# Kernel tuning notes

Measured on AMD Instinct MI355X. Metric: run time of the kernel, lower is better.

## Reference

```python
import jax, jax.numpy as jnp
import numpy as np

N, S, C = 2048, 14, 30  # batch, grid, channels (B=2 boxes*5 + 20 classes)
L_COORD, L_NOOBJ = 5.0, 0.5


def setup_inputs() -> dict:
    key = jax.random.key(0)
    k1, k2, k3 = jax.random.split(key, 3)
    pred = jax.random.uniform(k1, (N, S, S, C), minval=0.05, maxval=1.0, dtype=jnp.float32)
    target = jax.random.uniform(k2, (N, S, S, C), minval=0.05, maxval=1.0, dtype=jnp.float32)
    conf = (jax.random.uniform(k3, (N, S, S)) > 0.7).astype(jnp.float32)
    target = target.at[..., 4].set(conf)
    return {"pred": pred, "target": target}


def _to_xyxy(b):
    # b[..., :2] = center (grid units, divided by 14), b[..., 2:4] = w,h (image units)
    xy = b[..., :2] / 14.0
    wh = b[..., 2:4]
    return jnp.concatenate([xy - 0.5 * wh, xy + 0.5 * wh], axis=-1)


def _yolo_loss(pred, target):
    n = pred.shape[0]
    coo = (target[..., 4] > 0).astype(pred.dtype)   # [N,S,S] object mask
    noo = 1.0 - coo                                  # no-object mask
    pb = pred[..., :10].reshape(pred.shape[:3] + (2, 5))    # [N,S,S,2,5]
    tb = target[..., :10].reshape(target.shape[:3] + (2, 5))

    # IoU of the 2 predicted boxes vs the FIRST target box of the cell
    p_xy = _to_xyxy(pb)              # [N,S,S,2,4]
    t_xy = _to_xyxy(tb[..., 0, :])   # [N,S,S,4]
    lt = jnp.maximum(p_xy[..., :2], t_xy[..., None, :2])
    rb = jnp.minimum(p_xy[..., 2:], t_xy[..., None, 2:])
    wh = jnp.clip(rb - lt, 0.0)
    inter = wh[..., 0] * wh[..., 1]                          # [N,S,S,2]
    a1 = (p_xy[..., 2] - p_xy[..., 0]) * (p_xy[..., 3] - p_xy[..., 1])
    a2 = ((t_xy[..., 2] - t_xy[..., 0]) * (t_xy[..., 3] - t_xy[..., 1]))[..., None]
    iou = inter / (a1 + a2 - inter)

    # responsible box = argmax IoU (selection only; IoU value never enters the
    # loss because the original writes max_iou into cols :4 but reads col 4=0)
    r = jnp.argmax(jax.lax.stop_gradient(iou), axis=-1)      # [N,S,S]
    idx = r[..., None, None]
    resp_p = jnp.take_along_axis(pb, idx, axis=3)[..., 0, :]      # [N,S,S,5]
    resp_t = jnp.take_along_axis(tb, idx, axis=3)[..., 0, :]
    nresp_p = jnp.take_along_axis(pb, 1 - idx, axis=3)[..., 0, :]

    cm = coo[..., None]
    loc = jnp.sum(cm * (resp_p[..., :2] - resp_t[..., :2]) ** 2) \
        + jnp.sum(cm * (jnp.sqrt(resp_p[..., 2:4]) - jnp.sqrt(resp_t[..., 2:4])) ** 2)
    contain = jnp.sum(coo * resp_p[..., 4] ** 2)       # target IoU col 4 is 0 in original
    not_contain = jnp.sum(coo * nresp_p[..., 4] ** 2)  # target conf zeroed in original
    noobj = jnp.sum(noo * ((pred[..., 4] - target[..., 4]) ** 2
                           + (pred[..., 9] - target[..., 9]) ** 2))
    cls = jnp.sum(cm * (pred[..., 10:] - target[..., 10:]) ** 2)
    return (L_COORD * loc + 2.0 * contain + not_contain + L_NOOBJ * noobj + cls) / n


def reference(pred, target):
    return _yolo_loss(pred, target)
```

## Files before the change

### kernel.cpp

```cpp
#include <hip/hip_runtime.h>


constexpr int N_IMG = 2048;
constexpr int NC    = 30;
constexpr int CELLS = N_IMG * 14 * 14;
constexpr int BLOCK = 256;
constexpr int CPB   = 256;
constexpr int GRID  = CELLS / CPB;

__global__ __launch_bounds__(BLOCK)
void yolo_partial(const float* __restrict__ pred,
                  const float* __restrict__ targ,
                  float* __restrict__ partial)
{
    __shared__ float sp[CPB * NC];
    __shared__ float st[CPB * NC];
    __shared__ float wsum[BLOCK / 64];

    const int tid = threadIdx.x;
    const size_t base = (size_t)blockIdx.x * (size_t)(CPB * NC);

    const float4* gp = reinterpret_cast<const float4*>(pred + base);
    const float4* gt = reinterpret_cast<const float4*>(targ + base);
    float4* lp = reinterpret_cast<float4*>(sp);
    float4* lt = reinterpret_cast<float4*>(st);
    constexpr int NV = CPB * NC / 4;
    #pragma unroll
    for (int i = 0; i < NV / BLOCK; ++i) {
        lp[tid + i * BLOCK] = gp[tid + i * BLOCK];
        lt[tid + i * BLOCK] = gt[tid + i * BLOCK];
    }
    if (tid < NV - (NV / BLOCK) * BLOCK) {
        const int i = (NV / BLOCK) * BLOCK + tid;
        lp[i] = gp[i];
        lt[i] = gt[i];
    }
    __syncthreads();

    float pv[NC], tv[NC];
    {
        const float2* p2 = reinterpret_cast<const float2*>(sp + tid * NC);
        const float2* t2 = reinterpret_cast<const float2*>(st + tid * NC);
        #pragma unroll
        for (int i = 0; i < NC / 2; ++i) {
            float2 a = p2[i]; pv[2*i] = a.x; pv[2*i+1] = a.y;
            float2 b = t2[i]; tv[2*i] = b.x; tv[2*i+1] = b.y;
        }
    }

    const float coo = (tv[4] > 0.0f) ? 1.0f : 0.0f;

    const float txc = tv[0] / 14.0f, tyc = tv[1] / 14.0f;
    const float tx1 = txc - 0.5f * tv[2], ty1 = tyc - 0.5f * tv[3];
    const float tx2 = txc + 0.5f * tv[2], ty2 = tyc + 0.5f * tv[3];
    const float t_area = (tx2 - tx1) * (ty2 - ty1);

    float iou0, iou1;
    {
        const float xc = pv[0] / 14.0f, yc = pv[1] / 14.0f;
        const float x1 = xc - 0.5f * pv[2], y1 = yc - 0.5f * pv[3];
        const float x2 = xc + 0.5f * pv[2], y2 = yc + 0.5f * pv[3];
        const float a1 = (x2 - x1) * (y2 - y1);
        const float wx = fmaxf(fminf(x2, tx2) - fmaxf(x1, tx1), 0.0f);
        const float wy = fmaxf(fminf(y2, ty2) - fmaxf(y1, ty1), 0.0f);
        const float inter = wx * wy;
        iou0 = inter / (a1 + t_area - inter);
    }
    {
        const float xc = pv[5] / 14.0f, yc = pv[6] / 14.0f;
        const float x1 = xc - 0.5f * pv[7], y1 = yc - 0.5f * pv[8];
        const float x2 = xc + 0.5f * pv[7], y2 = yc + 0.5f * pv[8];
        const float a1 = (x2 - x1) * (y2 - y1);
        const float wx = fmaxf(fminf(x2, tx2) - fmaxf(x1, tx1), 0.0f);
        const float wy = fmaxf(fminf(y2, ty2) - fmaxf(y1, ty1), 0.0f);
        const float inter = wx * wy;
        iou1 = inter / (a1 + t_area - inter);
    }

    const bool sel = iou1 > iou0;
    const float rp0 = sel ? pv[5] : pv[0];
    const float rp1 = sel ? pv[6] : pv[1];
    const float rp2 = sel ? pv[7] : pv[2];
    const float rp3 = sel ? pv[8] : pv[3];
    const float rp4 = sel ? pv[9] : pv[4];
    const float rt0 = sel ? tv[5] : tv[0];
    const float rt1 = sel ? tv[6] : tv[1];
    const float rt2 = sel ? tv[7] : tv[2];
    const float rt3 = sel ? tv[8] : tv[3];
    const float nrp4 = sel ? pv[4] : pv[9];

    const float d0 = rp0 - rt0, d1 = rp1 - rt1;
    const float d2 = sqrtf(rp2) - sqrtf(rt2);
    const float d3 = sqrtf(rp3) - sqrtf(rt3);
    const float loc     = d0*d0 + d1*d1 + d2*d2 + d3*d3;
    const float contain = rp4 * rp4;
    const float notc    = nrp4 * nrp4;
    const float e4 = pv[4] - tv[4], e9 = pv[9] - tv[9];
    const float noobj = e4*e4 + e9*e9;
    float cls = 0.0f;
    #pragma unroll
    for (int c = 10; c < NC; ++c) { const float d = pv[c] - tv[c]; cls += d*d; }

    float cell = coo * (5.0f * loc + 2.0f * contain + notc + cls)
               + (1.0f - coo) * (0.5f * noobj);

    #pragma unroll
    for (int o = 32; o > 0; o >>= 1) cell += __shfl_down(cell, o, 64);
    if ((tid & 63) == 0) wsum[tid >> 6] = cell;
    __syncthreads();
    if (tid == 0)
        partial[blockIdx.x] = wsum[0] + wsum[1] + wsum[2] + wsum[3];
}

__global__ __launch_bounds__(256)
void yolo_final(const float* __restrict__ partial, float* __restrict__ out)
{
    const int tid = threadIdx.x;
    double s = 0.0;
    for (int i = tid; i < GRID; i += 256) s += (double)partial[i];
    #pragma unroll
    for (int o = 32; o > 0; o >>= 1) s += __shfl_down(s, o, 64);
    __shared__ double w[4];
    if ((tid & 63) == 0) w[tid >> 6] = s;
    __syncthreads();
    if (tid == 0) out[0] = (float)((w[0] + w[1] + w[2] + w[3]) / (double)N_IMG);
}

extern "C" void kernel_launch(void* const* d_in, const int* in_sizes, int n_in,
                              void* d_out, int out_size, void* d_ws, size_t ws_size,
                              hipStream_t stream)
{
    const float* pred = (const float*)d_in[0];
    const float* targ = (const float*)d_in[1];
    float* out        = (float*)d_out;
    float* partial    = (float*)d_ws;

    yolo_partial<<<GRID, BLOCK, 0, stream>>>(pred, targ, partial);
    yolo_final<<<1, 256, 0, stream>>>(partial, out);
}
```

Before: 24.21 us.

## Load cells directly from global memory instead of staging through LDS

Removes the shared-memory staging of each block's pred/target tiles and has each thread read its own 30-float cell straight from global memory with float2 loads. Division by 14 is also replaced with multiplication by a precomputed reciprocal. This drops about 60 KB of LDS per block and a barrier, which may raise occupancy. In exchange, each thread's loads are strided by 120 bytes, so global accesses are uncoalesced and rely on the caches to absorb the overfetch.

```diff
diff --git a/kernel.cpp b/kernel.cpp
--- a/kernel.cpp
+++ b/kernel.cpp
@@ -5,42 +5,21 @@
 constexpr int NC    = 30;
 constexpr int CELLS = N_IMG * 14 * 14;
 constexpr int BLOCK = 256;
-constexpr int CPB   = 256;
-constexpr int GRID  = CELLS / CPB;
+constexpr int GRID  = CELLS / BLOCK;
+constexpr float INV14 = 1.0f / 14.0f;
 
 __global__ __launch_bounds__(BLOCK)
-void yolo_partial(const float* __restrict__ pred,
-                  const float* __restrict__ targ,
-                  float* __restrict__ partial)
+void yolo_cell(const float* __restrict__ pred,
+               const float* __restrict__ targ,
+               float* __restrict__ partial)
 {
-    __shared__ float sp[CPB * NC];
-    __shared__ float st[CPB * NC];
-    __shared__ float wsum[BLOCK / 64];
-
-    const int tid = threadIdx.x;
-    const size_t base = (size_t)blockIdx.x * (size_t)(CPB * NC);
-
-    const float4* gp = reinterpret_cast<const float4*>(pred + base);
-    const float4* gt = reinterpret_cast<const float4*>(targ + base);
-    float4* lp = reinterpret_cast<float4*>(sp);
-    float4* lt = reinterpret_cast<float4*>(st);
-    constexpr int NV = CPB * NC / 4;
-    #pragma unroll
-    for (int i = 0; i < NV / BLOCK; ++i) {
-        lp[tid + i * BLOCK] = gp[tid + i * BLOCK];
-        lt[tid + i * BLOCK] = gt[tid + i * BLOCK];
-    }
-    if (tid < NV - (NV / BLOCK) * BLOCK) {
-        const int i = (NV / BLOCK) * BLOCK + tid;
-        lp[i] = gp[i];
-        lt[i] = gt[i];
-    }
-    __syncthreads();
+    const int tid  = threadIdx.x;
+    const int cell = blockIdx.x * BLOCK + tid;
 
     float pv[NC], tv[NC];
     {
-        const float2* p2 = reinterpret_cast<const float2*>(sp + tid * NC);
-        const float2* t2 = reinterpret_cast<const float2*>(st + tid * NC);
+        const float2* p2 = reinterpret_cast<const float2*>(pred + (size_t)cell * NC);
+        const float2* t2 = reinterpret_cast<const float2*>(targ + (size_t)cell * NC);
         #pragma unroll
         for (int i = 0; i < NC / 2; ++i) {
             float2 a = p2[i]; pv[2*i] = a.x; pv[2*i+1] = a.y;
@@ -50,14 +29,14 @@
 
     const float coo = (tv[4] > 0.0f) ? 1.0f : 0.0f;
 
-    const float txc = tv[0] / 14.0f, tyc = tv[1] / 14.0f;
+    const float txc = tv[0] * INV14, tyc = tv[1] * INV14;
     const float tx1 = txc - 0.5f * tv[2], ty1 = tyc - 0.5f * tv[3];
     const float tx2 = txc + 0.5f * tv[2], ty2 = tyc + 0.5f * tv[3];
     const float t_area = (tx2 - tx1) * (ty2 - ty1);
 
     float iou0, iou1;
     {
-        const float xc = pv[0] / 14.0f, yc = pv[1] / 14.0f;
+        const float xc = pv[0] * INV14, yc = pv[1] * INV14;
         const float x1 = xc - 0.5f * pv[2], y1 = yc - 0.5f * pv[3];
         const float x2 = xc + 0.5f * pv[2], y2 = yc + 0.5f * pv[3];
         const float a1 = (x2 - x1) * (y2 - y1);
@@ -67,7 +46,7 @@
         iou0 = inter / (a1 + t_area - inter);
     }
     {
-        const float xc = pv[5] / 14.0f, yc = pv[6] / 14.0f;
+        const float xc = pv[5] * INV14, yc = pv[6] * INV14;
         const float x1 = xc - 0.5f * pv[7], y1 = yc - 0.5f * pv[8];
         const float x2 = xc + 0.5f * pv[7], y2 = yc + 0.5f * pv[8];
         const float a1 = (x2 - x1) * (y2 - y1);
@@ -101,12 +80,13 @@
     #pragma unroll
     for (int c = 10; c < NC; ++c) { const float d = pv[c] - tv[c]; cls += d*d; }
 
-    float cell = coo * (5.0f * loc + 2.0f * contain + notc + cls)
-               + (1.0f - coo) * (0.5f * noobj);
+    float cellv = coo * (5.0f * loc + 2.0f * contain + notc + cls)
+                + (1.0f - coo) * (0.5f * noobj);
 
+    __shared__ float wsum[BLOCK / 64];
     #pragma unroll
-    for (int o = 32; o > 0; o >>= 1) cell += __shfl_down(cell, o, 64);
-    if ((tid & 63) == 0) wsum[tid >> 6] = cell;
+    for (int o = 32; o > 0; o >>= 1) cellv += __shfl_down(cellv, o, 64);
+    if ((tid & 63) == 0) wsum[tid >> 6] = cellv;
     __syncthreads();
     if (tid == 0)
         partial[blockIdx.x] = wsum[0] + wsum[1] + wsum[2] + wsum[3];
@@ -135,6 +115,6 @@
     float* out        = (float*)d_out;
     float* partial    = (float*)d_ws;
 
-    yolo_partial<<<GRID, BLOCK, 0, stream>>>(pred, targ, partial);
+    yolo_cell<<<GRID, BLOCK, 0, stream>>>(pred, targ, partial);
     yolo_final<<<1, 256, 0, stream>>>(partial, out);
 }
```

After: 31.03 us. 28.2% more time.
